# Kernel tuning notes

Hardware: AMD Instinct MI355X
Metric: run time of the kernel (lower is better)

## Reference

```python
import jax, jax.numpy as jnp
import numpy as np

D_MODEL = 1024
H = 16
D_H = D_MODEL // H


def setup_inputs() -> dict:
    key = jax.random.key(0)
    ks = jax.random.split(key, 10)
    B, T_dec, T_enc = 2, 2048, 2048
    s = 1.0 / np.sqrt(D_MODEL)
    return {
        "tgt": jax.random.normal(ks[0], (B, T_dec, D_MODEL), jnp.float32),
        "memory": jax.random.normal(ks[1], (B, T_enc, D_MODEL), jnp.float32),
        "W_q": jax.random.normal(ks[2], (D_MODEL, D_MODEL), jnp.float32) * s,
        "b_q": jnp.zeros((D_MODEL,), jnp.float32),
        "W_k": jax.random.normal(ks[3], (D_MODEL, D_MODEL), jnp.float32) * s,
        "b_k": jnp.zeros((D_MODEL,), jnp.float32),
        "W_v": jax.random.normal(ks[4], (D_MODEL, D_MODEL), jnp.float32) * s,
        "b_v": jnp.zeros((D_MODEL,), jnp.float32),
        "W_o": jax.random.normal(ks[5], (D_MODEL, D_MODEL), jnp.float32) * s,
        "b_o": jnp.zeros((D_MODEL,), jnp.float32),
    }


def reference(tgt, memory, W_q, b_q, W_k, b_k, W_v, b_v, W_o, b_o):
    B, T_dec, _ = tgt.shape
    T_enc = memory.shape[1]
    # Projections (nn.Linear: x @ W^T + b; here W stored as (in,out) so x @ W + b)
    Q = tgt @ W_q + b_q          # (B, T_dec, d_model)
    K = memory @ W_k + b_k       # (B, T_enc, d_model)
    V = memory @ W_v + b_v       # (B, T_enc, d_model)
    # split heads: (B, h, T, d_h)
    Q = Q.reshape(B, T_dec, H, D_H).transpose(0, 2, 1, 3)
    K = K.reshape(B, T_enc, H, D_H).transpose(0, 2, 1, 3)
    V = V.reshape(B, T_enc, H, D_H).transpose(0, 2, 1, 3)
    # scores (B, h, T_dec, T_enc)
    S = jnp.einsum("bhqd,bhkd->bhqk", Q, K) / jnp.sqrt(jnp.float32(D_H)).astype(Q.dtype)
    A = jax.nn.softmax(S, axis=-1)
    Y = jnp.einsum("bhqk,bhkd->bhqd", A, V)
    Y = Y.transpose(0, 2, 1, 3).reshape(B, T_dec, D_MODEL)
    return Y @ W_o + b_o
```

## Files before the change

kernel.cpp:

```cpp
#include <hip/hip_runtime.h>
#include <hip/hip_bf16.h>
#include <stdint.h>

typedef unsigned short u16;
typedef __attribute__((ext_vector_type(8))) short bf16x8;
typedef __attribute__((ext_vector_type(4))) short bf16x4;
typedef __attribute__((ext_vector_type(4))) float f32x4;

__device__ __forceinline__ float bf2f(u16 u) {
    union { unsigned int i; float f; } v; v.i = ((unsigned int)u) << 16; return v.f;
}
__device__ __forceinline__ u16 f2bf(float f) {
    union { float f; unsigned int i; } v; v.f = f;
    unsigned int x = v.i;
    return (u16)((x + 0x7fffu + ((x >> 16) & 1u)) >> 16);
}
__device__ __forceinline__ unsigned fbits(float f) {
    union { float f; unsigned int i; } v; v.f = f; return v.i;
}
__device__ __forceinline__ void async16(const void* g, void* lds) {
    __builtin_amdgcn_global_load_lds((const __attribute__((address_space(1))) void*)g,
                                     (__attribute__((address_space(3))) void*)lds,
                                     16, 0, 0);
}

#define QSCALE 0.18033688f

__global__ __launch_bounds__(256) void prep(
    const float* __restrict__ tgt, const float* __restrict__ mem,
    const float* __restrict__ Wq, const float* __restrict__ Wk,
    const float* __restrict__ Wv, const float* __restrict__ Wo,
    u16* __restrict__ Wt, u16* __restrict__ tgtb, u16* __restrict__ memb)
{
    __shared__ u16 tile[64][65];
    const int id = blockIdx.x;
    const int tid = threadIdx.x;
    if (id < 1024) {
        const int z = id >> 8;
        const float* in = (z == 0) ? Wq : (z == 1) ? Wk : (z == 2) ? Wv : Wo;
        u16* out = Wt + (size_t)z * 1048576;
        const int k0 = (id & 15) * 64, n0 = ((id >> 4) & 15) * 64;
        const int r = tid >> 2, c0 = (tid & 3) << 4;
#pragma unroll
        for (int i = 0; i < 4; ++i) {
            float4 v = *(const float4*)&in[(size_t)(k0 + r) * 1024 + n0 + c0 + i * 4];
            tile[c0 + i * 4 + 0][r] = f2bf(v.x);
            tile[c0 + i * 4 + 1][r] = f2bf(v.y);
            tile[c0 + i * 4 + 2][r] = f2bf(v.z);
            tile[c0 + i * 4 + 3][r] = f2bf(v.w);
        }
        __syncthreads();
#pragma unroll
        for (int i = 0; i < 2; ++i) {
            bf16x8 v;
#pragma unroll
            for (int j = 0; j < 8; ++j) v[j] = (short)tile[r][c0 + i * 8 + j];
            *(bf16x8*)&out[(size_t)(n0 + r) * 1024 + k0 + c0 + i * 8] = v;
        }
    } else {
        size_t i = ((size_t)(id - 1024) * 256 + tid) * 8;
        float4 a0 = *(const float4*)&tgt[i];
        float4 a1 = *(const float4*)&tgt[i + 4];
        float4 b0 = *(const float4*)&mem[i];
        float4 b1 = *(const float4*)&mem[i + 4];
        bf16x8 va, vb;
        va[0] = (short)f2bf(a0.x); va[1] = (short)f2bf(a0.y);
        va[2] = (short)f2bf(a0.z); va[3] = (short)f2bf(a0.w);
        va[4] = (short)f2bf(a1.x); va[5] = (short)f2bf(a1.y);
        va[6] = (short)f2bf(a1.z); va[7] = (short)f2bf(a1.w);
        vb[0] = (short)f2bf(b0.x); vb[1] = (short)f2bf(b0.y);
        vb[2] = (short)f2bf(b0.z); vb[3] = (short)f2bf(b0.w);
        vb[4] = (short)f2bf(b1.x); vb[5] = (short)f2bf(b1.y);
        vb[6] = (short)f2bf(b1.z); vb[7] = (short)f2bf(b1.w);
        *(bf16x8*)&tgtb[i] = va;
        *(bf16x8*)&memb[i] = vb;
    }
}

__global__ __launch_bounds__(256) void gemm_qkv(
    const u16* __restrict__ tgtb, const u16* __restrict__ memb,
    const u16* __restrict__ Wt,
    const float* __restrict__ bq, const float* __restrict__ bk, const float* __restrict__ bv,
    u16* __restrict__ Qb, u16* __restrict__ Kb, u16* __restrict__ Vtb)
{
    __shared__ __align__(16) u16 sA[128 * 32];
    __shared__ __align__(16) u16 sB[128 * 32];
    const int z = blockIdx.z;
    const u16* A = (z == 0) ? tgtb : memb;
    const u16* Bt = Wt + (size_t)z * 1048576;
    const float* bias = (z == 0) ? bq : (z == 1) ? bk : bv;

    const int tid = threadIdx.x;
    const int wave = tid >> 6, lane = tid & 63;
    const int quad = lane >> 4, l16 = lane & 15;
    const int m0 = blockIdx.x * 128, n0 = blockIdx.y * 128;
    const int wm = (wave & 1) * 64, wn = (wave >> 1) * 64;
    const int sw = (quad ^ ((l16 >> 1) & 3)) << 3;
    f32x4 acc[4][4] = {};

    for (int k0 = 0; k0 < 1024; k0 += 32) {
        __syncthreads();
#pragma unroll
        for (int r = 0; r < 2; ++r) {
            int c = tid + r * 256;
            int g = (c & 3) ^ ((c >> 3) & 3);
            const u16* gA = A + (size_t)(m0 + (c >> 2)) * 1024 + k0 + g * 8;
            async16(gA, (char*)sA + r * 4096 + wave * 1024);
            const u16* gB = Bt + (size_t)(n0 + (c >> 2)) * 1024 + k0 + g * 8;
            async16(gB, (char*)sB + r * 4096 + wave * 1024);
        }
        __syncthreads();
        bf16x8 af[4], bfr[4];
#pragma unroll
        for (int i = 0; i < 4; ++i) {
            af[i]  = *(const bf16x8*)&sA[(wm + i * 16 + l16) * 32 + sw];
            bfr[i] = *(const bf16x8*)&sB[(wn + i * 16 + l16) * 32 + sw];
        }
#pragma unroll
        for (int i = 0; i < 4; ++i)
#pragma unroll
            for (int j = 0; j < 4; ++j)
                acc[i][j] = __builtin_amdgcn_mfma_f32_16x16x32_bf16(af[i], bfr[j], acc[i][j], 0, 0, 0);
    }

    if (z == 2) {
#pragma unroll
        for (int j = 0; j < 4; ++j) {
            int n = n0 + wn + j * 16 + l16;
            float bb = bias[n];
            int d = n & 63;
#pragma unroll
            for (int i = 0; i < 4; ++i) {
                int mb = m0 + wm + i * 16 + quad * 4;
                int bh = (mb >> 11) * 16 + (n >> 6);
                bf16x4 pk;
#pragma unroll
                for (int r = 0; r < 4; ++r) pk[r] = (short)f2bf(acc[i][j][r] + bb);
                *(bf16x4*)&Vtb[(size_t)bh * 131072 + (size_t)d * 2048 + (mb & 2047)] = pk;
            }
        }
    } else {
        u16* C = (z == 0) ? Qb : Kb;
        const float scl = (z == 0) ? QSCALE : 1.0f;
#pragma unroll
        for (int j = 0; j < 4; ++j) {
            int n = n0 + wn + j * 16 + l16;
            float bb = bias[n];
#pragma unroll
            for (int i = 0; i < 4; ++i) {
                int mb = m0 + wm + i * 16 + quad * 4;
#pragma unroll
                for (int r = 0; r < 4; ++r)
                    C[(size_t)(mb + r) * 1024 + n] = f2bf((acc[i][j][r] + bb) * scl);
            }
        }
    }
}

__global__ __launch_bounds__(256) void gemm_out(
    const u16* __restrict__ A, const u16* __restrict__ Bt,
    const float* __restrict__ bias, float* __restrict__ C)
{
    __shared__ __align__(16) u16 sA[64 * 32];
    __shared__ __align__(16) u16 sB[128 * 32];
    const int tid = threadIdx.x;
    const int wave = tid >> 6, lane = tid & 63;
    const int quad = lane >> 4, l16 = lane & 15;
    const int m0 = blockIdx.x * 64, n0 = blockIdx.y * 128;
    const int wm = (wave & 1) * 32, wn = (wave >> 1) * 64;
    const int sw = (quad ^ ((l16 >> 1) & 3)) << 3;
    f32x4 acc[2][4] = {};

    for (int k0 = 0; k0 < 1024; k0 += 32) {
        __syncthreads();
        {
            int c = tid;
            int g = (c & 3) ^ ((c >> 3) & 3);
            const u16* gA = A + (size_t)(m0 + (c >> 2)) * 1024 + k0 + g * 8;
            async16(gA, (char*)sA + wave * 1024);
        }
#pragma unroll
        for (int r = 0; r < 2; ++r) {
            int c = tid + r * 256;
            int g = (c & 3) ^ ((c >> 3) & 3);
            const u16* gB = Bt + (size_t)(n0 + (c >> 2)) * 1024 + k0 + g * 8;
            async16(gB, (char*)sB + r * 4096 + wave * 1024);
        }
        __syncthreads();
        bf16x8 af[2], bfr[4];
#pragma unroll
        for (int i = 0; i < 2; ++i)
            af[i] = *(const bf16x8*)&sA[(wm + i * 16 + l16) * 32 + sw];
#pragma unroll
        for (int j = 0; j < 4; ++j)
            bfr[j] = *(const bf16x8*)&sB[(wn + j * 16 + l16) * 32 + sw];
#pragma unroll
        for (int i = 0; i < 2; ++i)
#pragma unroll
            for (int j = 0; j < 4; ++j)
                acc[i][j] = __builtin_amdgcn_mfma_f32_16x16x32_bf16(af[i], bfr[j], acc[i][j], 0, 0, 0);
    }
#pragma unroll
    for (int j = 0; j < 4; ++j) {
        int n = n0 + wn + j * 16 + l16;
        float bb = bias[n];
#pragma unroll
        for (int i = 0; i < 2; ++i) {
            int mb = m0 + wm + i * 16 + quad * 4;
#pragma unroll
            for (int r = 0; r < 4; ++r)
                C[(size_t)(mb + r) * 1024 + n] = acc[i][j][r] + bb;
        }
    }
}

__global__ __launch_bounds__(256, 4) void attn_kernel(
    const u16* __restrict__ Q,
    const u16* __restrict__ K,
    const u16* __restrict__ Vt,
    u16* __restrict__ Y)
{
    __shared__ __align__(16) u16 sK[2][4096];
    __shared__ __align__(16) u16 sV[2][4096];

    const int tid = threadIdx.x;
    const int wave = tid >> 6, lane = tid & 63;
    const int quad = lane >> 4, l16 = lane & 15;

    const int bidx = blockIdx.x;
    const int bh = (bidx & 7) * 4 + ((bidx >> 3) & 3);
    const int qt = bidx >> 5;
    const int b = bh >> 4, h = bh & 15;
    const size_t qrow0 = (size_t)b * 2048 + qt * 64;

    const size_t qrow = qrow0 + wave * 16 + l16;
    bf16x8 qf0 = *(const bf16x8*)&Q[qrow * 1024 + h * 64 + quad * 8];
    bf16x8 qf1 = *(const bf16x8*)&Q[qrow * 1024 + h * 64 + 32 + quad * 8];

    f32x4 oacc[4] = {};
    float rowacc = 0.0f;

    const u16* Kbase = K + (size_t)b * 2048 * 1024 + h * 64;
    const u16* Vbase = Vt + (size_t)bh * 131072;

    const int x7 = l16 & 7;
    int koff[4][2], voff[4][4];
#pragma unroll
    for (int ks = 0; ks < 4; ++ks)
#pragma unroll
        for (int kf = 0; kf < 2; ++kf)
            koff[ks][kf] = ((ks * 16 + l16) * 8 + ((kf * 4 + quad) ^ x7)) * 8;
#pragma unroll
    for (int mt = 0; mt < 4; ++mt)
#pragma unroll
        for (int ks = 0; ks < 4; ++ks)
            voff[mt][ks] = ((mt * 16 + l16) * 8 + ((ks * 2 + (quad >> 1)) ^ x7)) * 8 + (quad & 1) * 4;

    const int srow = tid >> 3;
    const int g0 = (tid & 7) ^ (srow & 7);
    const int g1 = (tid & 7) ^ ((srow + 32) & 7);

#define STAGE(kv0, buf)                                                          \
    {                                                                            \
        async16(Kbase + (size_t)((kv0) + srow) * 1024 + g0 * 8,                  \
                (char*)&sK[buf][0] + wave * 1024);                               \
        async16(Kbase + (size_t)((kv0) + srow + 32) * 1024 + g1 * 8,             \
                (char*)&sK[buf][0] + 4096 + wave * 1024);                        \
        async16(Vbase + (size_t)srow * 2048 + (kv0) + g0 * 8,                    \
                (char*)&sV[buf][0] + wave * 1024);                               \
        async16(Vbase + (size_t)(srow + 32) * 2048 + (kv0) + g1 * 8,             \
                (char*)&sV[buf][0] + 4096 + wave * 1024);                        \
    }

    STAGE(((qt & 31) * 64), 0);

    for (int i = 0; i < 32; ++i) {
        __syncthreads();
        if (i < 31) {
            int kvn = ((qt + i + 1) & 31) * 64;
            STAGE(kvn, (i + 1) & 1);
        }
        const u16* kb = &sK[i & 1][0];
        const u16* vb = &sV[i & 1][0];
#pragma unroll
        for (int ks = 0; ks < 4; ++ks) {
            bf16x8 kf0 = *(const bf16x8*)&kb[koff[ks][0]];
            bf16x8 kf1 = *(const bf16x8*)&kb[koff[ks][1]];
            f32x4 s = {0.f, 0.f, 0.f, 0.f};
            s = __builtin_amdgcn_mfma_f32_16x16x32_bf16(kf0, qf0, s, 0, 0, 0);
            s = __builtin_amdgcn_mfma_f32_16x16x32_bf16(kf1, qf1, s, 0, 0, 0);
            float p0 = __builtin_amdgcn_exp2f(s[0]);
            float p1 = __builtin_amdgcn_exp2f(s[1]);
            float p2 = __builtin_amdgcn_exp2f(s[2]);
            float p3 = __builtin_amdgcn_exp2f(s[3]);
            rowacc += (p0 + p1) + (p2 + p3);
            unsigned lo = __builtin_amdgcn_perm(fbits(p1) + 0x8000u, fbits(p0) + 0x8000u, 0x07060302u);
            unsigned hi = __builtin_amdgcn_perm(fbits(p3) + 0x8000u, fbits(p2) + 0x8000u, 0x07060302u);
            union { unsigned u[2]; bf16x4 v; } pku;
            pku.u[0] = lo; pku.u[1] = hi;
#pragma unroll
            for (int mt = 0; mt < 4; ++mt) {
                bf16x4 vv = *(const bf16x4*)&vb[voff[mt][ks]];
                oacc[mt] = __builtin_amdgcn_mfma_f32_16x16x16bf16_1k(vv, pku.v, oacc[mt], 0, 0, 0);
            }
        }
    }

    rowacc += __shfl_xor(rowacc, 16, 64);
    rowacc += __shfl_xor(rowacc, 32, 64);
    const float inv = 1.0f / rowacc;

#pragma unroll
    for (int mt = 0; mt < 4; ++mt) {
        bf16x4 o;
#pragma unroll
        for (int r = 0; r < 4; ++r) o[r] = (short)f2bf(oacc[mt][r] * inv);
        *(bf16x4*)&Y[qrow * 1024 + h * 64 + mt * 16 + quad * 4] = o;
    }
}

extern "C" void kernel_launch(void* const* d_in, const int* in_sizes, int n_in,
                              void* d_out, int out_size, void* d_ws, size_t ws_size,
                              hipStream_t stream) {
    const float* tgt = (const float*)d_in[0];
    const float* mem = (const float*)d_in[1];
    const float* Wq  = (const float*)d_in[2];
    const float* bq  = (const float*)d_in[3];
    const float* Wk  = (const float*)d_in[4];
    const float* bk  = (const float*)d_in[5];
    const float* Wv  = (const float*)d_in[6];
    const float* bv  = (const float*)d_in[7];
    const float* Wo  = (const float*)d_in[8];
    const float* bo  = (const float*)d_in[9];

    u16* ws = (u16*)d_ws;
    const size_t SZ = 4194304;
    u16* Wt   = ws;
    u16* tgtb = ws + 4 * SZ;
    u16* memb = tgtb + SZ;
    u16* Qb   = memb + SZ;
    u16* Kb   = Qb + SZ;
    u16* Vtb  = Kb + SZ;
    u16* Yb   = Vtb + SZ;
    float* out = (float*)d_out;

    prep<<<dim3(3072), 256, 0, stream>>>(tgt, mem, Wq, Wk, Wv, Wo, Wt, tgtb, memb);
    gemm_qkv<<<dim3(32, 8, 3), 256, 0, stream>>>(tgtb, memb, Wt, bq, bk, bv, Qb, Kb, Vtb);
    attn_kernel<<<dim3(1024), 256, 0, stream>>>(Qb, Kb, Vtb, Yb);
    gemm_out<<<dim3(64, 8), 256, 0, stream>>>(Yb, Wt + 3 * (size_t)1048576, bo, out);
}
```

Before: 228.1 us.

## Double-buffer LDS tiles in the projection GEMMs and stagger each block's K start

Both the QKV projection GEMM and the output projection GEMM now use two LDS buffers. The loads for the next K tile are issued right after the barrier, so they overlap the MFMA work on the current tile, and the loop needs one barrier per step instead of two. Each block also starts its K loop at a different tile offset that depends on its block index and wraps around. This is meant to spread concurrent global reads across addresses and cut contention. In exchange the GEMMs use twice the LDS and accumulate in a different order, which can change rounding slightly.

```diff
diff --git a/kernel.cpp b/kernel.cpp
--- a/kernel.cpp
+++ b/kernel.cpp
@@ -83,8 +83,8 @@
     const float* __restrict__ bq, const float* __restrict__ bk, const float* __restrict__ bv,
     u16* __restrict__ Qb, u16* __restrict__ Kb, u16* __restrict__ Vtb)
 {
-    __shared__ __align__(16) u16 sA[128 * 32];
-    __shared__ __align__(16) u16 sB[128 * 32];
+    __shared__ __align__(16) u16 sA[2][4096];
+    __shared__ __align__(16) u16 sB[2][4096];
     const int z = blockIdx.z;
     const u16* A = (z == 0) ? tgtb : memb;
     const u16* Bt = Wt + (size_t)z * 1048576;
@@ -96,32 +96,45 @@
     const int m0 = blockIdx.x * 128, n0 = blockIdx.y * 128;
     const int wm = (wave & 1) * 64, wn = (wave >> 1) * 64;
     const int sw = (quad ^ ((l16 >> 1) & 3)) << 3;
+    const int kt0 = (blockIdx.x + blockIdx.y * 4 + z * 11) & 31;
     f32x4 acc[4][4] = {};
 
-    for (int k0 = 0; k0 < 1024; k0 += 32) {
+    const int c0r = tid, c1r = tid + 256;
+    const int g0 = (c0r & 3) ^ ((c0r >> 3) & 3);
+    const int g1 = (c1r & 3) ^ ((c1r >> 3) & 3);
+    const size_t arow0 = (size_t)(m0 + (c0r >> 2)) * 1024 + g0 * 8;
+    const size_t arow1 = (size_t)(m0 + (c1r >> 2)) * 1024 + g1 * 8;
+    const size_t brow0 = (size_t)(n0 + (c0r >> 2)) * 1024 + g0 * 8;
+    const size_t brow1 = (size_t)(n0 + (c1r >> 2)) * 1024 + g1 * 8;
+
+#define QSTAGE(kt, buf)                                                      \
+    {                                                                        \
+        const int k0s = (kt) * 32;                                           \
+        async16(A + arow0 + k0s, (char*)&sA[buf][0] + wave * 1024);          \
+        async16(A + arow1 + k0s, (char*)&sA[buf][0] + 4096 + wave * 1024);   \
+        async16(Bt + brow0 + k0s, (char*)&sB[buf][0] + wave * 1024);         \
+        async16(Bt + brow1 + k0s, (char*)&sB[buf][0] + 4096 + wave * 1024);  \
+    }
+
+    QSTAGE(kt0, 0);
+    for (int i = 0; i < 32; ++i) {
         __syncthreads();
-#pragma unroll
-        for (int r = 0; r < 2; ++r) {
-            int c = tid + r * 256;
-            int g = (c & 3) ^ ((c >> 3) & 3);
-            const u16* gA = A + (size_t)(m0 + (c >> 2)) * 1024 + k0 + g * 8;
-            async16(gA, (char*)sA + r * 4096 + wave * 1024);
-            const u16* gB = Bt + (size_t)(n0 + (c >> 2)) * 1024 + k0 + g * 8;
-            async16(gB, (char*)sB + r * 4096 + wave * 1024);
-        }
-        __syncthreads();
+        if (i < 31) QSTAGE((kt0 + i + 1) & 31, (i + 1) & 1);
+        const u16* a = &sA[i & 1][0];
+        const u16* bb = &sB[i & 1][0];
         bf16x8 af[4], bfr[4];
 #pragma unroll
-        for (int i = 0; i < 4; ++i) {
-            af[i]  = *(const bf16x8*)&sA[(wm + i * 16 + l16) * 32 + sw];
-            bfr[i] = *(const bf16x8*)&sB[(wn + i * 16 + l16) * 32 + sw];
-        }
-#pragma unroll
-        for (int i = 0; i < 4; ++i)
+        for (int t = 0; t < 4; ++t) {
+            af[t]  = *(const bf16x8*)&a[(wm + t * 16 + l16) * 32 + sw];
+            bfr[t] = *(const bf16x8*)&bb[(wn + t * 16 + l16) * 32 + sw];
+        }
+#pragma unroll
+        for (int t = 0; t < 4; ++t)
 #pragma unroll
             for (int j = 0; j < 4; ++j)
-                acc[i][j] = __builtin_amdgcn_mfma_f32_16x16x32_bf16(af[i], bfr[j], acc[i][j], 0, 0, 0);
-    }
+                acc[t][j] = __builtin_amdgcn_mfma_f32_16x16x32_bf16(af[t], bfr[j], acc[t][j], 0, 0, 0);
+    }
+#undef QSTAGE
 
     if (z == 2) {
 #pragma unroll
@@ -161,45 +174,53 @@
     const u16* __restrict__ A, const u16* __restrict__ Bt,
     const float* __restrict__ bias, float* __restrict__ C)
 {
-    __shared__ __align__(16) u16 sA[64 * 32];
-    __shared__ __align__(16) u16 sB[128 * 32];
+    __shared__ __align__(16) u16 sA[2][2048];
+    __shared__ __align__(16) u16 sB[2][4096];
     const int tid = threadIdx.x;
     const int wave = tid >> 6, lane = tid & 63;
     const int quad = lane >> 4, l16 = lane & 15;
     const int m0 = blockIdx.x * 64, n0 = blockIdx.y * 128;
     const int wm = (wave & 1) * 32, wn = (wave >> 1) * 64;
     const int sw = (quad ^ ((l16 >> 1) & 3)) << 3;
+    const int kt0 = (blockIdx.x + blockIdx.y * 8) & 31;
     f32x4 acc[2][4] = {};
 
-    for (int k0 = 0; k0 < 1024; k0 += 32) {
+    const int c0r = tid, c1r = tid + 256;
+    const int g0 = (c0r & 3) ^ ((c0r >> 3) & 3);
+    const int g1 = (c1r & 3) ^ ((c1r >> 3) & 3);
+    const size_t arow0 = (size_t)(m0 + (c0r >> 2)) * 1024 + g0 * 8;
+    const size_t brow0 = (size_t)(n0 + (c0r >> 2)) * 1024 + g0 * 8;
+    const size_t brow1 = (size_t)(n0 + (c1r >> 2)) * 1024 + g1 * 8;
+
+#define OSTAGE(kt, buf)                                                      \
+    {                                                                        \
+        const int k0s = (kt) * 32;                                           \
+        async16(A + arow0 + k0s, (char*)&sA[buf][0] + wave * 1024);          \
+        async16(Bt + brow0 + k0s, (char*)&sB[buf][0] + wave * 1024);         \
+        async16(Bt + brow1 + k0s, (char*)&sB[buf][0] + 4096 + wave * 1024);  \
+    }
+
+    OSTAGE(kt0, 0);
+    for (int i = 0; i < 32; ++i) {
         __syncthreads();
-        {
-            int c = tid;
-            int g = (c & 3) ^ ((c >> 3) & 3);
-            const u16* gA = A + (size_t)(m0 + (c >> 2)) * 1024 + k0 + g * 8;
-            async16(gA, (char*)sA + wave * 1024);
-        }
-#pragma unroll
-        for (int r = 0; r < 2; ++r) {
-            int c = tid + r * 256;
-            int g = (c & 3) ^ ((c >> 3) & 3);
-            const u16* gB = Bt + (size_t)(n0 + (c >> 2)) * 1024 + k0 + g * 8;
-            async16(gB, (char*)sB + r * 4096 + wave * 1024);
-        }
-        __syncthreads();
+        if (i < 31) OSTAGE((kt0 + i + 1) & 31, (i + 1) & 1);
+        const u16* a = &sA[i & 1][0];
+        const u16* bb = &sB[i & 1][0];
         bf16x8 af[2], bfr[4];
 #pragma unroll
-        for (int i = 0; i < 2; ++i)
-            af[i] = *(const bf16x8*)&sA[(wm + i * 16 + l16) * 32 + sw];
+        for (int t = 0; t < 2; ++t)
+            af[t] = *(const bf16x8*)&a[(wm + t * 16 + l16) * 32 + sw];
 #pragma unroll
         for (int j = 0; j < 4; ++j)
-            bfr[j] = *(const bf16x8*)&sB[(wn + j * 16 + l16) * 32 + sw];
-#pragma unroll
-        for (int i = 0; i < 2; ++i)
+            bfr[j] = *(const bf16x8*)&bb[(wn + j * 16 + l16) * 32 + sw];
+#pragma unroll
+        for (int t = 0; t < 2; ++t)
 #pragma unroll
             for (int j = 0; j < 4; ++j)
-                acc[i][j] = __builtin_amdgcn_mfma_f32_16x16x32_bf16(af[i], bfr[j], acc[i][j], 0, 0, 0);
-    }
+                acc[t][j] = __builtin_amdgcn_mfma_f32_16x16x32_bf16(af[t], bfr[j], acc[t][j], 0, 0, 0);
+    }
+#undef OSTAGE
+
 #pragma unroll
     for (int j = 0; j < 4; ++j) {
         int n = n0 + wn + j * 16 + l16;
```

Result: slower. 235.9 us (+3.4%).
